# Kernel optimization log

Measured on AMD Instinct MI355X. Metric: run time of the kernel, lower is better.

## Reference

```python
import jax, jax.numpy as jnp
import numpy as np

N, E = 30000, 480000
HID, NB, D = 256, 128, 2
SW = D * D * NB        # struct-encoder width = bundle_dim^2 * num_bundles = 512
NL, NSAGE = 2, 5       # outer BDL layers, SAGE layers inside struct encoder
OUT = 5
EPS = 1e-5


def _gelu(x):
    return jax.nn.gelu(x, approximate=False)  # torch nn.GELU default (exact)


def _mean_agg(x, src, dst):
    # mean over incoming edges: agg[v] = mean_{u->v} x[u]
    s = jax.ops.segment_sum(x[src], dst, num_segments=N)
    deg = jax.ops.segment_sum(jnp.ones((E,), x.dtype), dst, num_segments=N)
    return s / jnp.maximum(deg, 1.0)[:, None]


def _layernorm(x, g, b):
    m = jnp.mean(x, -1, keepdims=True)
    v = jnp.mean((x - m) ** 2, -1, keepdims=True)
    return (x - m) * jax.lax.rsqrt(v + EPS) * g + b


def _householder(X):
    # torch.nn.utils.parametrizations Orthogonal, orthogonal_map='householder':
    # Q = H_0 H_1 ... H_{d-1}, H_i = I - tau_i v_i v_i^T, v_i = strict-lower col i with unit diag
    d = X.shape[-1]
    A = jnp.tril(X, k=-1)
    tau = 2.0 / (1.0 + jnp.sum(A * A, axis=-2))  # [M, d]
    eye = jnp.eye(d, dtype=X.dtype)
    Q = jnp.broadcast_to(eye, X.shape)
    for i in range(d):
        v = A[:, :, i] + eye[i]
        Qv = jnp.einsum('mij,mj->mi', Q, v)
        Q = Q - tau[:, i, None, None] * Qv[:, :, None] * v[:, None, :]
    return Q


def _struct_encoder(h, src, dst, se_in_w, se_in_b, sage_w1, sage_b1, sage_w2, sage_b2, se_out_w, se_out_b):
    # Model('SAGE', 5, ...) with normalization='None'; dropout inactive in eval
    z = _gelu(h @ se_in_w + se_in_b)
    for i in range(NSAGE):
        m = _mean_agg(z, src, dst)
        zc = jnp.concatenate([z, m], axis=-1)  # SAGE: cat(self, mean(neigh))
        z = z + (_gelu(zc @ sage_w1[i] + sage_b1[i]) @ sage_w2[i] + sage_b2[i])
    return z @ se_out_w + se_out_b


def _forward(x, w_in, b_in, se_in_w, se_in_b, sage_w1, sage_b1, sage_w2, sage_b2,
             se_out_w, se_out_b, enc_w1, enc_b1, enc_w2, enc_b2, ln_g, ln_b,
             bdl_w1, bdl_b1, bdl_w2, bdl_b2, out_ln_g, out_ln_b, w_out, b_out, edge_index):
    src, dst = edge_index[0], edge_index[1]
    h = _gelu(x @ w_in + b_in)
    for k in range(NL):
        enc = _struct_encoder(h, src, dst, se_in_w, se_in_b, sage_w1, sage_b1,
                              sage_w2, sage_b2, se_out_w, se_out_b)
        nr = _gelu(enc @ enc_w1[k] + enc_b1[k]) @ enc_w2[k] + enc_b2[k]  # [N, SW]
        O = _householder(nr.reshape(N * NB, D, D)).reshape(N, NB, D, D)
        # BDL residual module: transport features through per-node bundle frames
        hn = _layernorm(h, ln_g[k], ln_b[k])
        hb = hn.reshape(N, NB, D)
        y = jnp.einsum('nbij,nbj->nbi', O, hb)                       # rotate into frame
        agg = _mean_agg(y.reshape(N, NB * D), src, dst).reshape(N, NB, D)
        msg = jnp.einsum('nbji,nbj->nbi', O, agg).reshape(N, NB * D)  # O^T transports back
        hc = jnp.concatenate([hn, msg], axis=-1)
        h = h + (_gelu(hc @ bdl_w1[k] + bdl_b1[k]) @ bdl_w2[k] + bdl_b2[k])
    h = _layernorm(h, out_ln_g, out_ln_b)
    return h @ w_out + b_out  # [N, OUT]; .squeeze(1) is a no-op for OUT>1


def _w(key, fan_in, shape):
    return jax.random.normal(key, shape, dtype=jnp.float32) / np.sqrt(fan_in)


def setup_inputs() -> dict:
    key = jax.random.key(0)
    ks = iter(jax.random.split(key, 40))
    f32 = jnp.float32
    return {
        'x': jax.random.normal(next(ks), (N, HID), dtype=f32),
        'edge_index': jax.random.randint(next(ks), (2, E), 0, N, dtype=jnp.int32),
        'w_in': _w(next(ks), HID, (HID, HID)), 'b_in': jnp.zeros((HID,), f32),
        'se_in_w': _w(next(ks), HID, (HID, SW)), 'se_in_b': jnp.zeros((SW,), f32),
        'sage_w1': _w(next(ks), 2 * SW, (NSAGE, 2 * SW, SW)), 'sage_b1': jnp.zeros((NSAGE, SW), f32),
        'sage_w2': _w(next(ks), SW, (NSAGE, SW, SW)), 'sage_b2': jnp.zeros((NSAGE, SW), f32),
        'se_out_w': _w(next(ks), SW, (SW, SW)), 'se_out_b': jnp.zeros((SW,), f32),
        'enc_w1': _w(next(ks), SW, (NL, SW, SW)), 'enc_b1': jnp.zeros((NL, SW), f32),
        'enc_w2': _w(next(ks), SW, (NL, SW, SW)), 'enc_b2': jnp.zeros((NL, SW), f32),
        'ln_g': jnp.ones((NL, HID), f32), 'ln_b': jnp.zeros((NL, HID), f32),
        'bdl_w1': _w(next(ks), 2 * HID, (NL, 2 * HID, HID)), 'bdl_b1': jnp.zeros((NL, HID), f32),
        'bdl_w2': _w(next(ks), HID, (NL, HID, HID)), 'bdl_b2': jnp.zeros((NL, HID), f32),
        'out_ln_g': jnp.ones((HID,), f32), 'out_ln_b': jnp.zeros((HID,), f32),
        'w_out': _w(next(ks), HID, (HID, OUT)), 'b_out': jnp.zeros((OUT,), f32),
    }


def reference(x, edge_index, w_in, b_in, se_in_w, se_in_b, sage_w1, sage_b1, sage_w2, sage_b2,
              se_out_w, se_out_b, enc_w1, enc_b1, enc_w2, enc_b2, ln_g, ln_b,
              bdl_w1, bdl_b1, bdl_w2, bdl_b2, out_ln_g, out_ln_b, w_out, b_out):
    return _forward(x, w_in, b_in, se_in_w, se_in_b, sage_w1, sage_b1, sage_w2, sage_b2,
                    se_out_w, se_out_b, enc_w1, enc_b1, enc_w2, enc_b2, ln_g, ln_b,
                    bdl_w1, bdl_b1, bdl_w2, bdl_b2, out_ln_g, out_ln_b, w_out, b_out, edge_index)
```

## Files before the change

### kernel.cpp

```cpp
#include <hip/hip_runtime.h>
#include <hip/hip_bf16.h>
#include <cstdint>
#include <cstddef>


typedef __attribute__((ext_vector_type(8))) short short8;
typedef __attribute__((ext_vector_type(4))) float f32x4;

__device__ __forceinline__ float gelu_exact(float x) {
  return 0.5f * x * (1.0f + erff(x * 0.7071067811865475f));
}
__device__ __forceinline__ unsigned short f2bf(float f) {
  __hip_bfloat16 b = __float2bfloat16(f);
  return *reinterpret_cast<unsigned short*>(&b);
}
__device__ __forceinline__ float bf2f(unsigned short u) {
  return __uint_as_float((unsigned)u << 16);
}
__device__ __forceinline__ float bflo(unsigned u) { return __uint_as_float(u << 16); }
__device__ __forceinline__ float bfhi(unsigned u) { return __uint_as_float(u & 0xffff0000u); }
__device__ __forceinline__ unsigned packbf(float f0, float f1) {
  return (unsigned)f2bf(f0) | ((unsigned)f2bf(f1) << 16);
}
__device__ __forceinline__ void gload16(const void* g, void* l) {
  __builtin_amdgcn_global_load_lds((const __attribute__((address_space(1))) void*)g,
                                   (__attribute__((address_space(3))) void*)l, 16, 0, 0);
}
#define SCHEDB() __builtin_amdgcn_sched_barrier(0)

__global__ void k_hist(const int* __restrict__ dst, int* __restrict__ deg, int E) {
  int i = blockIdx.x * 256 + threadIdx.x;
  if (i < E) atomicAdd(&deg[dst[i]], 1);
}

__global__ __launch_bounds__(1024)
void k_scan(const int* __restrict__ deg, int* __restrict__ rp, int* __restrict__ cur, int Nn) {
  __shared__ int part[1024];
  int t = threadIdx.x;
  int chunk = (Nn + 1023) >> 10;
  int s0 = t * chunk;
  int e0 = s0 + chunk; if (e0 > Nn) e0 = Nn;
  int s = 0;
  for (int i = s0; i < e0; ++i) s += deg[i];
  part[t] = s;
  __syncthreads();
  for (int off = 1; off < 1024; off <<= 1) {
    int v = (t >= off) ? part[t - off] : 0;
    __syncthreads();
    part[t] += v;
    __syncthreads();
  }
  int base = (t == 0) ? 0 : part[t - 1];
  for (int i = s0; i < e0; ++i) {
    rp[i] = base; cur[i] = base; base += deg[i];
  }
  if (t == 0) rp[Nn] = part[1023];
}

__global__ void k_fill(const int* __restrict__ src, const int* __restrict__ dst,
                       int* __restrict__ cur, int* __restrict__ srcs, int E) {
  int i = blockIdx.x * 256 + threadIdx.x;
  if (i < E) {
    int p = atomicAdd(&cur[dst[i]], 1);
    srcs[p] = src[i];
  }
}

__global__ void k_wT(const float* __restrict__ W, unsigned short* __restrict__ Wt, int K, int Nc) {
  const float* Ws = W + (size_t)blockIdx.y * K * Nc;
  unsigned short* Wd = Wt + (size_t)blockIdx.y * K * Nc;
  int idx = blockIdx.x * 256 + threadIdx.x;
  if (idx >= K * Nc) return;
  int k = idx % K, n = idx / K;
  Wd[(size_t)n * K + k] = f2bf(Ws[(size_t)k * Nc + n]);
}

__global__ void k_cast(const float* __restrict__ src, unsigned short* __restrict__ dst, int n) {
  int i = blockIdx.x * 256 + threadIdx.x;
  if (i < n) dst[i] = f2bf(src[i]);
}

template<int ACT, int RES, bool DUAL, bool W32, bool WBF, bool OP>
__global__ __launch_bounds__(256)
void k_mfma(const unsigned short* __restrict__ A1, const unsigned short* __restrict__ A2,
            int K1, int K2,
            const unsigned short* __restrict__ Wt, const float* __restrict__ bias,
            const float* R32, const unsigned short* Rbf,
            float* C32, unsigned short* Cbf, float* Op, int M, int Nc) {
  const int mb_cnt = (M + 127) >> 7;
  const int nb_cnt = Nc >> 7;
  int u = blockIdx.x;
  int xcd = u & 7;
  int rest = u >> 3;
  int nb = rest % nb_cnt;
  int mb = (rest / nb_cnt) * 8 + xcd;
  if (mb >= mb_cnt) return;
  const int m0 = mb << 7, n0 = nb << 7;

  __shared__ unsigned short As[2][128 * 64];
  __shared__ unsigned short Bs[2][128 * 64];
  const int tid = threadIdx.x;
  const int lane = tid & 63, wv = tid >> 6;
  const int wr = (wv >> 1) * 64, wc = (wv & 1) * 64;
  const int rA = lane & 15, kg = lane >> 4;
  const int Ktot = K1 + K2;
  const int nt = Ktot >> 6;

  f32x4 acc[4][4];
#pragma unroll
  for (int m = 0; m < 4; ++m)
#pragma unroll
    for (int n = 0; n < 4; ++n)
#pragma unroll
      for (int r = 0; r < 4; ++r) acc[m][n][r] = 0.f;

  auto stage = [&](int t, int b) {
    int k0 = t << 6;
    const unsigned short* Asrc; int kc, lda;
    if (!DUAL || k0 < K1) { Asrc = A1; kc = k0; lda = K1; }
    else                  { Asrc = A2; kc = k0 - K1; lda = K2; }
#pragma unroll
    for (int is = 0; is < 4; ++is) {
      int chunk = is * 256 + tid;
      int row = chunk >> 3, seg = chunk & 7;
      int ks = seg ^ (row & 7);
      int gm = m0 + row; gm = gm < M ? gm : M - 1;
      gload16(Asrc + (size_t)gm * lda + kc + ks * 8, (char*)As[b] + (size_t)chunk * 16);
      gload16(Wt + (size_t)(n0 + row) * Ktot + k0 + ks * 8, (char*)Bs[b] + (size_t)chunk * 16);
    }
  };

  stage(0, 0);
  if (nt > 1) stage(1, 1);

  for (int t = 0; t < nt; ++t) {
    const int b = t & 1;
    if (t + 1 < nt) asm volatile("s_waitcnt vmcnt(8)" ::: "memory");
    else            asm volatile("s_waitcnt vmcnt(0)" ::: "memory");
    SCHEDB();
    __builtin_amdgcn_s_barrier();
    SCHEDB();

    short8 af[2][4], bq[2][4];
#pragma unroll
    for (int kk = 0; kk < 2; ++kk) {
#pragma unroll
      for (int m = 0; m < 4; ++m) {
        int row = wr + m * 16 + rA;
        int ks = (kk * 4 + kg) ^ (row & 7);
        af[kk][m] = *reinterpret_cast<const short8*>((const char*)As[b] + row * 128 + ks * 16);
      }
#pragma unroll
      for (int n = 0; n < 4; ++n) {
        int col = wc + n * 16 + rA;
        int ks = (kk * 4 + kg) ^ (col & 7);
        bq[kk][n] = *reinterpret_cast<const short8*>((const char*)Bs[b] + col * 128 + ks * 16);
      }
    }
    asm volatile("s_waitcnt lgkmcnt(0)" ::: "memory");
    SCHEDB();
    __builtin_amdgcn_s_barrier();
    SCHEDB();
    if (t + 2 < nt) stage(t + 2, b);

    __builtin_amdgcn_s_setprio(1);
#pragma unroll
    for (int kk = 0; kk < 2; ++kk)
#pragma unroll
      for (int m = 0; m < 4; ++m)
#pragma unroll
        for (int n = 0; n < 4; ++n)
          acc[m][n] = __builtin_amdgcn_mfma_f32_16x16x32_bf16(af[kk][m], bq[kk][n],
                                                              acc[m][n], 0, 0, 0);
    __builtin_amdgcn_s_setprio(0);
  }

#pragma unroll
  for (int m = 0; m < 4; ++m) {
    int gr0 = m0 + wr + m * 16 + kg * 4;
#pragma unroll
    for (int n = 0; n < 4; ++n) {
      int gc = n0 + wc + n * 16 + rA;
      float bv = bias[gc];
#pragma unroll
      for (int r = 0; r < 4; ++r) {
        int gr = gr0 + r;
        if (gr < M) {
          float v = acc[m][n][r] + bv;
          if (ACT == 1) v = gelu_exact(v);
          if (RES == 1) v += R32[(size_t)gr * Nc + gc];
          if (RES == 2) v += bf2f(Rbf[(size_t)gr * Nc + gc]);
          if (W32) C32[(size_t)gr * Nc + gc] = v;
          if (WBF) Cbf[(size_t)gr * Nc + gc] = f2bf(v);
          if (OP) {
            if ((rA & 3) == 2) {
              float iv = 1.0f / (1.0f + v * v);
              float* op = Op + (size_t)gr * 256 + ((gc >> 2) << 1);
              op[0] = (v * v - 1.0f) * iv;
              op[1] = 2.0f * v * iv;
            }
          }
        }
      }
    }
  }
}

template<int W, bool ROT>
__global__ __launch_bounds__(256)
void k_agg(const unsigned short* __restrict__ X, const int* __restrict__ rp,
           const int* __restrict__ srcs, const float* __restrict__ o,
           unsigned short* __restrict__ out, int Nn) {
  int wid = (blockIdx.x * 256 + threadIdx.x) >> 6;
  int lane = threadIdx.x & 63;
  if (wid >= Nn) return;
  constexpr int PE = W / 64;
  float a[PE];
#pragma unroll
  for (int p = 0; p < PE; ++p) a[p] = 0.f;
  int beg = rp[wid], end = rp[wid + 1];
  for (int e = beg; e < end; ++e) {
    int s = srcs[e];
    const unsigned* row = reinterpret_cast<const unsigned*>(X + (size_t)s * W) + lane * (PE / 2);
    if (PE == 8) {
      uint4 v = *reinterpret_cast<const uint4*>(row);
      a[0] += bflo(v.x); a[1] += bfhi(v.x); a[2] += bflo(v.y); a[3] += bfhi(v.y);
      a[4] += bflo(v.z); a[5] += bfhi(v.z); a[6] += bflo(v.w); a[7] += bfhi(v.w);
    } else {
      uint2 v = *reinterpret_cast<const uint2*>(row);
      a[0] += bflo(v.x); a[1] += bfhi(v.x); a[2] += bflo(v.y); a[3] += bfhi(v.y);
    }
  }
  float inv = (end > beg) ? 1.0f / (float)(end - beg) : 0.0f;
#pragma unroll
  for (int p = 0; p < PE; ++p) a[p] *= inv;
  if (ROT) {
    float4 oc = *reinterpret_cast<const float4*>(o + (size_t)wid * 256 + lane * 4);
    float m0 = oc.x * a[0] - oc.y * a[1];
    float m1 = oc.y * a[0] + oc.x * a[1];
    float m2 = oc.z * a[2] - oc.w * a[3];
    float m3 = oc.w * a[2] + oc.z * a[3];
    a[0] = m0; a[1] = m1; a[2] = m2; a[3] = m3;
  }
  unsigned short* op = out + (size_t)wid * W + lane * PE;
  if (PE == 8) {
    uint4 rv;
    rv.x = packbf(a[0], a[1]); rv.y = packbf(a[2], a[3]);
    rv.z = packbf(a[4], a[5]); rv.w = packbf(a[6], a[7]);
    *reinterpret_cast<uint4*>(op) = rv;
  } else {
    uint2 rv;
    rv.x = packbf(a[0], a[1]); rv.y = packbf(a[2], a[3]);
    *reinterpret_cast<uint2*>(op) = rv;
  }
}

__global__ __launch_bounds__(256)
void k_ln_rot(const float* __restrict__ h, const float* __restrict__ o,
              const float* __restrict__ g, const float* __restrict__ b,
              unsigned short* __restrict__ hn, unsigned short* __restrict__ y, int Nn) {
  int wid = (blockIdx.x * 256 + threadIdx.x) >> 6;
  int lane = threadIdx.x & 63;
  if (wid >= Nn) return;
  float4 v = reinterpret_cast<const float4*>(h + (size_t)wid * 256)[lane];
  float s = v.x + v.y + v.z + v.w;
  float ss = v.x * v.x + v.y * v.y + v.z * v.z + v.w * v.w;
#pragma unroll
  for (int off = 1; off < 64; off <<= 1) { s += __shfl_xor(s, off); ss += __shfl_xor(ss, off); }
  float mean = s * (1.0f / 256.0f);
  float var = ss * (1.0f / 256.0f) - mean * mean;
  float rs = rsqrtf(var + 1e-5f);
  float4 gg = reinterpret_cast<const float4*>(g)[lane];
  float4 bb = reinterpret_cast<const float4*>(b)[lane];
  float h0 = (v.x - mean) * rs * gg.x + bb.x;
  float h1 = (v.y - mean) * rs * gg.y + bb.y;
  float h2 = (v.z - mean) * rs * gg.z + bb.z;
  float h3 = (v.w - mean) * rs * gg.w + bb.w;
  uint2 hv; hv.x = packbf(h0, h1); hv.y = packbf(h2, h3);
  *reinterpret_cast<uint2*>(hn + (size_t)wid * 256 + lane * 4) = hv;
  float4 oc = *reinterpret_cast<const float4*>(o + (size_t)wid * 256 + lane * 4);
  float y0 =  oc.x * h0 + oc.y * h1;
  float y1 = -oc.y * h0 + oc.x * h1;
  float y2 =  oc.z * h2 + oc.w * h3;
  float y3 = -oc.w * h2 + oc.z * h3;
  uint2 yv; yv.x = packbf(y0, y1); yv.y = packbf(y2, y3);
  *reinterpret_cast<uint2*>(y + (size_t)wid * 256 + lane * 4) = yv;
}

__global__ __launch_bounds__(256)
void k_final(const float* __restrict__ h, const float* __restrict__ g,
             const float* __restrict__ b, const float* __restrict__ wout,
             const float* __restrict__ bout, float* __restrict__ out, int Nn) {
  int wid = (blockIdx.x * 256 + threadIdx.x) >> 6;
  int lane = threadIdx.x & 63;
  if (wid >= Nn) return;
  float4 v = reinterpret_cast<const float4*>(h + (size_t)wid * 256)[lane];
  float s = v.x + v.y + v.z + v.w;
  float ss = v.x * v.x + v.y * v.y + v.z * v.z + v.w * v.w;
#pragma unroll
  for (int off = 1; off < 64; off <<= 1) { s += __shfl_xor(s, off); ss += __shfl_xor(ss, off); }
  float mean = s * (1.0f / 256.0f);
  float var = ss * (1.0f / 256.0f) - mean * mean;
  float rs = rsqrtf(var + 1e-5f);
  float4 gg = reinterpret_cast<const float4*>(g)[lane];
  float4 bb = reinterpret_cast<const float4*>(b)[lane];
  float hv[4];
  hv[0] = (v.x - mean) * rs * gg.x + bb.x;
  hv[1] = (v.y - mean) * rs * gg.y + bb.y;
  hv[2] = (v.z - mean) * rs * gg.z + bb.z;
  hv[3] = (v.w - mean) * rs * gg.w + bb.w;
  int c0 = lane * 4;
  float dots[5];
#pragma unroll
  for (int j = 0; j < 5; ++j) {
    float p = hv[0] * wout[(size_t)(c0 + 0) * 5 + j] + hv[1] * wout[(size_t)(c0 + 1) * 5 + j]
            + hv[2] * wout[(size_t)(c0 + 2) * 5 + j] + hv[3] * wout[(size_t)(c0 + 3) * 5 + j];
#pragma unroll
    for (int off = 1; off < 64; off <<= 1) p += __shfl_xor(p, off);
    dots[j] = p;
  }
  if (lane == 0) {
#pragma unroll
    for (int j = 0; j < 5; ++j) out[(size_t)wid * 5 + j] = dots[j] + bout[j];
  }
}

extern "C" void kernel_launch(void* const* d_in, const int* in_sizes, int n_in,
                              void* d_out, int out_size, void* d_ws, size_t ws_size,
                              hipStream_t stream) {
  const float* x       = (const float*)d_in[0];
  const int*   ei      = (const int*)  d_in[1];
  const float* w_in    = (const float*)d_in[2];
  const float* b_in    = (const float*)d_in[3];
  const float* se_in_w = (const float*)d_in[4];
  const float* se_in_b = (const float*)d_in[5];
  const float* sage_w1 = (const float*)d_in[6];
  const float* sage_b1 = (const float*)d_in[7];
  const float* sage_w2 = (const float*)d_in[8];
  const float* sage_b2 = (const float*)d_in[9];
  const float* se_out_w= (const float*)d_in[10];
  const float* se_out_b= (const float*)d_in[11];
  const float* enc_w1  = (const float*)d_in[12];
  const float* enc_b1  = (const float*)d_in[13];
  const float* enc_w2  = (const float*)d_in[14];
  const float* enc_b2  = (const float*)d_in[15];
  const float* ln_g    = (const float*)d_in[16];
  const float* ln_b    = (const float*)d_in[17];
  const float* bdl_w1  = (const float*)d_in[18];
  const float* bdl_b1  = (const float*)d_in[19];
  const float* bdl_w2  = (const float*)d_in[20];
  const float* bdl_b2  = (const float*)d_in[21];
  const float* oln_g   = (const float*)d_in[22];
  const float* oln_b   = (const float*)d_in[23];
  const float* w_out   = (const float*)d_in[24];
  const float* b_out   = (const float*)d_in[25];
  float* out = (float*)d_out;

  const int HID = 256, SW = 512;
  const int N = in_sizes[0] / HID;
  const int E = in_sizes[1] / 2;

  float* ws = (float*)d_ws;
  float* h32 = ws;
  float* o   = h32 + (size_t)N * HID;
  unsigned short* h_bf = (unsigned short*)(o + (size_t)N * HID);
  unsigned short* z_bf = h_bf + (size_t)N * HID;
  unsigned short* t_bf = z_bf + (size_t)N * SW;
  unsigned short* u_bf = t_bf + (size_t)N * SW;
  unsigned short* wts = u_bf + (size_t)N * SW;
  size_t off = 0;
  unsigned short* wt_in    = wts + off; off += 256 * 256;
  unsigned short* wt_se_in = wts + off; off += 512 * 256;
  unsigned short* wt_sage1 = wts + off; off += (size_t)5 * 512 * 1024;
  unsigned short* wt_sage2 = wts + off; off += (size_t)5 * 512 * 512;
  unsigned short* wt_se_out= wts + off; off += 512 * 512;
  unsigned short* wt_enc1  = wts + off; off += (size_t)2 * 512 * 512;
  unsigned short* wt_enc2  = wts + off; off += (size_t)2 * 512 * 512;
  unsigned short* wt_bdl1  = wts + off; off += (size_t)2 * 256 * 512;
  unsigned short* wt_bdl2  = wts + off; off += (size_t)2 * 256 * 256;
  int* deg  = (int*)(wts + off);
  int* rp   = deg + N;
  int* cur  = rp + N + 1;
  int* srcs = cur + N;
  size_t need = (size_t)((char*)(srcs + E) - (char*)d_ws);
  if (ws_size < need) return;

  unsigned short* xbf = u_bf;
  unsigned short* hn  = z_bf;
  unsigned short* y   = z_bf + (size_t)N * HID;
  unsigned short* msg = t_bf;
  unsigned short* g2  = u_bf;

  const int* esrc = ei;
  const int* edst = ei + E;

  auto cdiv = [](int a, int b) { return (a + b - 1) / b; };
  dim3 blk(256);
  int mb_cnt = cdiv(N, 128);
  int mgrp = cdiv(mb_cnt, 8);
  int g_g256 = mgrp * 8 * 2;
  int g_g512 = mgrp * 8 * 4;
  int gw = cdiv(N * 64, 256);

  hipMemsetAsync(deg, 0, sizeof(int) * N, stream);
  k_hist<<<cdiv(E, 256), blk, 0, stream>>>(edst, deg, E);
  k_scan<<<1, 1024, 0, stream>>>(deg, rp, cur, N);
  k_fill<<<cdiv(E, 256), blk, 0, stream>>>(esrc, edst, cur, srcs, E);

  auto wT = [&](const float* W, unsigned short* Wt, int K, int Nc, int cnt) {
    k_wT<<<dim3(cdiv(K * Nc, 256), cnt), blk, 0, stream>>>(W, Wt, K, Nc);
  };
  wT(w_in, wt_in, 256, 256, 1);
  wT(se_in_w, wt_se_in, 256, 512, 1);
  wT(sage_w1, wt_sage1, 1024, 512, 5);
  wT(sage_w2, wt_sage2, 512, 512, 5);
  wT(se_out_w, wt_se_out, 512, 512, 1);
  wT(enc_w1, wt_enc1, 512, 512, 2);
  wT(enc_w2, wt_enc2, 512, 512, 2);
  wT(bdl_w1, wt_bdl1, 512, 256, 2);
  wT(bdl_w2, wt_bdl2, 256, 256, 2);
  k_cast<<<cdiv(N * HID, 256), blk, 0, stream>>>(x, xbf, N * HID);

  k_mfma<1, 0, false, true, true, false><<<g_g256, blk, 0, stream>>>(
      xbf, nullptr, 256, 0, wt_in, b_in, nullptr, nullptr, h32, h_bf, nullptr, N, 256);

  for (int k = 0; k < 2; ++k) {
    k_mfma<1, 0, false, false, true, false><<<g_g512, blk, 0, stream>>>(
        h_bf, nullptr, 256, 0, wt_se_in, se_in_b, nullptr, nullptr, nullptr, z_bf, nullptr, N, 512);
    for (int i = 0; i < 5; ++i) {
      k_agg<512, false><<<gw, blk, 0, stream>>>(z_bf, rp, srcs, nullptr, t_bf, N);
      k_mfma<1, 0, true, false, true, false><<<g_g512, blk, 0, stream>>>(
          z_bf, t_bf, 512, 512, wt_sage1 + (size_t)i * 512 * 1024,
          sage_b1 + (size_t)i * SW, nullptr, nullptr, nullptr, u_bf, nullptr, N, 512);
      k_mfma<0, 2, false, false, true, false><<<g_g512, blk, 0, stream>>>(
          u_bf, nullptr, 512, 0, wt_sage2 + (size_t)i * 512 * 512,
          sage_b2 + (size_t)i * SW, nullptr, z_bf, nullptr, z_bf, nullptr, N, 512);
    }
    k_mfma<0, 0, false, false, true, false><<<g_g512, blk, 0, stream>>>(
        z_bf, nullptr, 512, 0, wt_se_out, se_out_b, nullptr, nullptr, nullptr, t_bf, nullptr, N, 512);
    k_mfma<1, 0, false, false, true, false><<<g_g512, blk, 0, stream>>>(
        t_bf, nullptr, 512, 0, wt_enc1 + (size_t)k * 512 * 512,
        enc_b1 + (size_t)k * SW, nullptr, nullptr, nullptr, u_bf, nullptr, N, 512);
    k_mfma<0, 0, false, false, false, true><<<g_g512, blk, 0, stream>>>(
        u_bf, nullptr, 512, 0, wt_enc2 + (size_t)k * 512 * 512,
        enc_b2 + (size_t)k * SW, nullptr, nullptr, nullptr, nullptr, o, N, 512);
    k_ln_rot<<<gw, blk, 0, stream>>>(h32, o, ln_g + (size_t)k * HID, ln_b + (size_t)k * HID, hn, y, N);
    k_agg<256, true><<<gw, blk, 0, stream>>>(y, rp, srcs, o, msg, N);
    k_mfma<1, 0, true, false, true, false><<<g_g256, blk, 0, stream>>>(
        hn, msg, 256, 256, wt_bdl1 + (size_t)k * 256 * 512,
        bdl_b1 + (size_t)k * HID, nullptr, nullptr, nullptr, g2, nullptr, N, 256);
    k_mfma<0, 1, false, true, true, false><<<g_g256, blk, 0, stream>>>(
        g2, nullptr, 256, 0, wt_bdl2 + (size_t)k * 256 * 256,
        bdl_b2 + (size_t)k * HID, h32, nullptr, h32, h_bf, nullptr, N, 256);
  }

  k_final<<<gw, blk, 0, stream>>>(h32, oln_g, oln_b, w_out, b_out, out, N);
}
```

Measured before the change: 2.610 ms.

## Fold struct-encoder output projection into first encoder linear; unroll edge aggregation

Because se_out and enc_w1 are consecutive linear maps with no nonlinearity between them, the two weights are pre-multiplied once per call (W_se_out·W_enc1) and the bias is folded through, removing one N×512×512 GEMM per outer layer. The fused weight is computed with the existing MFMA kernel on the transposed weights, and a small kernel computes the fused bias. Separately, the neighbor-mean aggregation loop is unrolled by four edges to keep more gathers in flight. The fused weight is rounded to bf16, which changes rounding slightly compared with two separate bf16 GEMMs.

```diff
diff --git a/kernel.cpp b/kernel.cpp
--- a/kernel.cpp
+++ b/kernel.cpp
@@ -78,6 +78,17 @@
 __global__ void k_cast(const float* __restrict__ src, unsigned short* __restrict__ dst, int n) {
   int i = blockIdx.x * 256 + threadIdx.x;
   if (i < n) dst[i] = f2bf(src[i]);
+}
+
+__global__ void k_bfuse(const float* __restrict__ b_so, const float* __restrict__ W_e1,
+                        const float* __restrict__ b_e1, float* __restrict__ bf) {
+  int k = blockIdx.y;
+  int n = blockIdx.x * 256 + threadIdx.x;
+  if (n >= 512) return;
+  const float* W = W_e1 + (size_t)k * 512 * 512;
+  float s = b_e1[(size_t)k * 512 + n];
+  for (int e = 0; e < 512; ++e) s += b_so[e] * W[(size_t)e * 512 + n];
+  bf[(size_t)k * 512 + n] = s;
 }
 
 template<int ACT, int RES, bool DUAL, bool W32, bool WBF, bool OP>
@@ -219,15 +230,44 @@
 #pragma unroll
   for (int p = 0; p < PE; ++p) a[p] = 0.f;
   int beg = rp[wid], end = rp[wid + 1];
-  for (int e = beg; e < end; ++e) {
-    int s = srcs[e];
-    const unsigned* row = reinterpret_cast<const unsigned*>(X + (size_t)s * W) + lane * (PE / 2);
-    if (PE == 8) {
-      uint4 v = *reinterpret_cast<const uint4*>(row);
+  int e = beg;
+  if (PE == 8) {
+    for (; e + 4 <= end; e += 4) {
+      int s0 = srcs[e], s1 = srcs[e + 1], s2 = srcs[e + 2], s3 = srcs[e + 3];
+      uint4 v0 = *reinterpret_cast<const uint4*>(X + (size_t)s0 * W + lane * 8);
+      uint4 v1 = *reinterpret_cast<const uint4*>(X + (size_t)s1 * W + lane * 8);
+      uint4 v2 = *reinterpret_cast<const uint4*>(X + (size_t)s2 * W + lane * 8);
+      uint4 v3 = *reinterpret_cast<const uint4*>(X + (size_t)s3 * W + lane * 8);
+      a[0] += bflo(v0.x) + bflo(v1.x) + bflo(v2.x) + bflo(v3.x);
+      a[1] += bfhi(v0.x) + bfhi(v1.x) + bfhi(v2.x) + bfhi(v3.x);
+      a[2] += bflo(v0.y) + bflo(v1.y) + bflo(v2.y) + bflo(v3.y);
+      a[3] += bfhi(v0.y) + bfhi(v1.y) + bfhi(v2.y) + bfhi(v3.y);
+      a[4] += bflo(v0.z) + bflo(v1.z) + bflo(v2.z) + bflo(v3.z);
+      a[5] += bfhi(v0.z) + bfhi(v1.z) + bfhi(v2.z) + bfhi(v3.z);
+      a[6] += bflo(v0.w) + bflo(v1.w) + bflo(v2.w) + bflo(v3.w);
+      a[7] += bfhi(v0.w) + bfhi(v1.w) + bfhi(v2.w) + bfhi(v3.w);
+    }
+    for (; e < end; ++e) {
+      int s = srcs[e];
+      uint4 v = *reinterpret_cast<const uint4*>(X + (size_t)s * W + lane * 8);
       a[0] += bflo(v.x); a[1] += bfhi(v.x); a[2] += bflo(v.y); a[3] += bfhi(v.y);
       a[4] += bflo(v.z); a[5] += bfhi(v.z); a[6] += bflo(v.w); a[7] += bfhi(v.w);
-    } else {
-      uint2 v = *reinterpret_cast<const uint2*>(row);
+    }
+  } else {
+    for (; e + 4 <= end; e += 4) {
+      int s0 = srcs[e], s1 = srcs[e + 1], s2 = srcs[e + 2], s3 = srcs[e + 3];
+      uint2 v0 = *reinterpret_cast<const uint2*>(X + (size_t)s0 * W + lane * 4);
+      uint2 v1 = *reinterpret_cast<const uint2*>(X + (size_t)s1 * W + lane * 4);
+      uint2 v2 = *reinterpret_cast<const uint2*>(X + (size_t)s2 * W + lane * 4);
+      uint2 v3 = *reinterpret_cast<const uint2*>(X + (size_t)s3 * W + lane * 4);
+      a[0] += bflo(v0.x) + bflo(v1.x) + bflo(v2.x) + bflo(v3.x);
+      a[1] += bfhi(v0.x) + bfhi(v1.x) + bfhi(v2.x) + bfhi(v3.x);
+      a[2] += bflo(v0.y) + bflo(v1.y) + bflo(v2.y) + bflo(v3.y);
+      a[3] += bfhi(v0.y) + bfhi(v1.y) + bfhi(v2.y) + bfhi(v3.y);
+    }
+    for (; e < end; ++e) {
+      int s = srcs[e];
+      uint2 v = *reinterpret_cast<const uint2*>(X + (size_t)s * W + lane * 4);
       a[0] += bflo(v.x); a[1] += bfhi(v.x); a[2] += bflo(v.y); a[3] += bfhi(v.y);
     }
   }
@@ -373,11 +413,14 @@
   unsigned short* wt_se_in = wts + off; off += 512 * 256;
   unsigned short* wt_sage1 = wts + off; off += (size_t)5 * 512 * 1024;
   unsigned short* wt_sage2 = wts + off; off += (size_t)5 * 512 * 512;
-  unsigned short* wt_se_out= wts + off; off += 512 * 512;
+  unsigned short* so_bf    = wts + off; off += 512 * 512;
   unsigned short* wt_enc1  = wts + off; off += (size_t)2 * 512 * 512;
   unsigned short* wt_enc2  = wts + off; off += (size_t)2 * 512 * 512;
   unsigned short* wt_bdl1  = wts + off; off += (size_t)2 * 256 * 512;
   unsigned short* wt_bdl2  = wts + off; off += (size_t)2 * 256 * 256;
+  unsigned short* wt_f     = wts + off; off += (size_t)2 * 512 * 512;
+  float* bf_f = (float*)(wts + off); off += 2 * 512 * 2;
+  float* zb   = (float*)(wts + off); off += 512 * 2;
   int* deg  = (int*)(wts + off);
   int* rp   = deg + N;
   int* cur  = rp + N + 1;
@@ -400,6 +443,7 @@
   int mgrp = cdiv(mb_cnt, 8);
   int g_g256 = mgrp * 8 * 2;
   int g_g512 = mgrp * 8 * 4;
+  int g_F    = 1 * 8 * 4;
   int gw = cdiv(N * 64, 256);
 
   hipMemsetAsync(deg, 0, sizeof(int) * N, stream);
@@ -414,12 +458,18 @@
   wT(se_in_w, wt_se_in, 256, 512, 1);
   wT(sage_w1, wt_sage1, 1024, 512, 5);
   wT(sage_w2, wt_sage2, 512, 512, 5);
-  wT(se_out_w, wt_se_out, 512, 512, 1);
   wT(enc_w1, wt_enc1, 512, 512, 2);
   wT(enc_w2, wt_enc2, 512, 512, 2);
   wT(bdl_w1, wt_bdl1, 512, 256, 2);
   wT(bdl_w2, wt_bdl2, 256, 256, 2);
+  k_cast<<<cdiv(512 * 512, 256), blk, 0, stream>>>(se_out_w, so_bf, 512 * 512);
   k_cast<<<cdiv(N * HID, 256), blk, 0, stream>>>(x, xbf, N * HID);
+  hipMemsetAsync(zb, 0, 512 * sizeof(float), stream);
+  k_bfuse<<<dim3(2, 2), blk, 0, stream>>>(se_out_b, enc_w1, enc_b1, bf_f);
+  for (int k = 0; k < 2; ++k)
+    k_mfma<0, 0, false, false, true, false><<<g_F, blk, 0, stream>>>(
+        wt_enc1 + (size_t)k * 512 * 512, nullptr, 512, 0, so_bf, zb,
+        nullptr, nullptr, nullptr, wt_f + (size_t)k * 512 * 512, nullptr, 512, 512);
 
   k_mfma<1, 0, false, true, true, false><<<g_g256, blk, 0, stream>>>(
       xbf, nullptr, 256, 0, wt_in, b_in, nullptr, nullptr, h32, h_bf, nullptr, N, 256);
@@ -436,11 +486,9 @@
           u_bf, nullptr, 512, 0, wt_sage2 + (size_t)i * 512 * 512,
           sage_b2 + (size_t)i * SW, nullptr, z_bf, nullptr, z_bf, nullptr, N, 512);
     }
-    k_mfma<0, 0, false, false, true, false><<<g_g512, blk, 0, stream>>>(
-        z_bf, nullptr, 512, 0, wt_se_out, se_out_b, nullptr, nullptr, nullptr, t_bf, nullptr, N, 512);
     k_mfma<1, 0, false, false, true, false><<<g_g512, blk, 0, stream>>>(
-        t_bf, nullptr, 512, 0, wt_enc1 + (size_t)k * 512 * 512,
-        enc_b1 + (size_t)k * SW, nullptr, nullptr, nullptr, u_bf, nullptr, N, 512);
+        z_bf, nullptr, 512, 0, wt_f + (size_t)k * 512 * 512,
+        bf_f + (size_t)k * 512, nullptr, nullptr, nullptr, u_bf, nullptr, N, 512);
     k_mfma<0, 0, false, false, false, true><<<g_g512, blk, 0, stream>>>(
         u_bf, nullptr, 512, 0, wt_enc2 + (size_t)k * 512 * 512,
         enc_b2 + (size_t)k * SW, nullptr, nullptr, nullptr, nullptr, o, N, 512);
```

Measured after the change: 2.499 ms. -4.3%, faster.
